# Kernel tuning notes

Measured on AMD Instinct MI355X. Metric: run time of the kernel, lower is better.

The kernel has to match this reference:

```python
import jax, jax.numpy as jnp
import numpy as np

N = 100000      # nodes
E = 1600000     # directed edges (before self-loops)
DIN = 128       # input feature dim
HID = 32        # per-head hidden dim
HEADS = 4
D1 = HID * HEADS  # 128, concat width
NG = 64         # graphs in batch
NEG_SLOPE = 0.2 # PyG GATConv leaky_relu slope


def setup_inputs() -> dict:
    key = jax.random.key(0)
    ks = jax.random.split(key, 16)
    s = 0.05
    x = jax.random.normal(ks[0], (N, DIN), dtype=jnp.float32)
    edge_index = jax.random.randint(ks[1], (2, E), 0, N, dtype=jnp.int32)
    batch = jnp.sort(jax.random.randint(ks[2], (N,), 0, NG, dtype=jnp.int32))
    # GATConv 1: in=DIN, out=HID, heads=HEADS, concat=True
    W1 = jax.random.normal(ks[3], (D1, DIN), dtype=jnp.float32) * s
    a1s = jax.random.normal(ks[4], (HEADS, HID), dtype=jnp.float32) * s
    a1d = jax.random.normal(ks[5], (HEADS, HID), dtype=jnp.float32) * s
    b1 = jnp.zeros((D1,), jnp.float32)
    # GATConv 2: in=D1, out=HID, heads=HEADS, concat=True
    W2 = jax.random.normal(ks[6], (D1, D1), dtype=jnp.float32) * s
    a2s = jax.random.normal(ks[7], (HEADS, HID), dtype=jnp.float32) * s
    a2d = jax.random.normal(ks[8], (HEADS, HID), dtype=jnp.float32) * s
    b2 = jnp.zeros((D1,), jnp.float32)
    # GATConv 3: in=D1, out=HID, heads=HEADS, concat=False (mean over heads)
    W3 = jax.random.normal(ks[9], (D1, D1), dtype=jnp.float32) * s
    a3s = jax.random.normal(ks[10], (HEADS, HID), dtype=jnp.float32) * s
    a3d = jax.random.normal(ks[11], (HEADS, HID), dtype=jnp.float32) * s
    b3 = jnp.zeros((HID,), jnp.float32)
    lin_w = jax.random.normal(ks[12], (1, HID), dtype=jnp.float32) * s
    lin_b = jnp.zeros((1,), jnp.float32)
    return {"x": x, "edge_index": edge_index, "batch": batch,
            "W1": W1, "a1s": a1s, "a1d": a1d, "b1": b1,
            "W2": W2, "a2s": a2s, "a2d": a2d, "b2": b2,
            "W3": W3, "a3s": a3s, "a3d": a3d, "b3": b3,
            "lin_w": lin_w, "lin_b": lin_b}


def _gat_conv(x, ei, W, att_src, att_dst, bias, concat):
    """PyG GATConv (no edge features, self-loops already in ei)."""
    n = x.shape[0]
    h = (x @ W.T).reshape(n, HEADS, HID)          # [N, H, C]
    src, dst = ei[0], ei[1]
    a_src = jnp.einsum('nhc,hc->nh', h, att_src)  # [N, H]
    a_dst = jnp.einsum('nhc,hc->nh', h, att_dst)
    e = jax.nn.leaky_relu(a_src[src] + a_dst[dst], NEG_SLOPE)  # [Etot, H]
    # segment softmax over incoming edges of each dst node
    e_max = jax.ops.segment_max(e, dst, num_segments=n)
    ex = jnp.exp(e - e_max[dst])
    denom = jax.ops.segment_sum(ex, dst, num_segments=n)
    alpha = ex / denom[dst]                        # [Etot, H]
    out = jax.ops.segment_sum(h[src] * alpha[:, :, None], dst, num_segments=n)
    if concat:
        out = out.reshape(n, HEADS * HID)
    else:
        out = out.mean(axis=1)
    return out + bias


def reference(x, edge_index, batch, W1, a1s, a1d, b1, W2, a2s, a2d, b2,
              W3, a3s, a3d, b3, lin_w, lin_b):
    loops = jnp.arange(N, dtype=edge_index.dtype)
    ei = jnp.concatenate([edge_index, jnp.stack([loops, loops])], axis=1)
    h = jax.nn.elu(_gat_conv(x, ei, W1, a1s, a1d, b1, True))
    h = jax.nn.elu(_gat_conv(h, ei, W2, a2s, a2d, b2, True))
    h = jax.nn.elu(_gat_conv(h, ei, W3, a3s, a3d, b3, False))
    h = h @ lin_w.T + lin_b                        # [N, 1]
    counts = jax.ops.segment_sum(jnp.ones((N,), h.dtype), batch, num_segments=NG)
    pooled = jax.ops.segment_sum(h, batch, num_segments=NG) / counts[:, None]
    return pooled.squeeze()                        # [NG]
```

## Files before the change

### kernel.cpp

```cpp
#include <hip/hip_runtime.h>
#include <hip/hip_fp16.h>
#include <math.h>

#define D1 128
#define NEG 0.2f
#define NODE_SHIFT 9
#define BIN_NODES 512
#define MAXBIN 256

typedef _Float16 v8h __attribute__((ext_vector_type(8)));
typedef float v4f __attribute__((ext_vector_type(4)));

__device__ __forceinline__ float lrelu(float v){ return v > 0.f ? v : NEG * v; }
__device__ __forceinline__ float elu_f(float v){ return v > 0.f ? v : __expf(v) - 1.f; }

__device__ __forceinline__ unsigned f2h2(float a, float b){
    return ((unsigned)__half_as_ushort(__float2half_rn(b)) << 16) |
           (unsigned)__half_as_ushort(__float2half_rn(a));
}
__device__ __forceinline__ float2 h2f2(unsigned u){
    float lo = __half2float(__ushort_as_half((unsigned short)(u & 0xffffu)));
    float hi = __half2float(__ushort_as_half((unsigned short)(u >> 16)));
    return make_float2(lo, hi);
}


__global__ __launch_bounds__(256) void kb_hist(const int* __restrict__ ei,
                                               int* __restrict__ binCnt,
                                               int n_edges, int etot, int nbin){
    __shared__ int h[MAXBIN];
    for (int i = threadIdx.x; i < nbin; i += 256) h[i] = 0;
    __syncthreads();
    int stride = gridDim.x * 256;
    for (int e = blockIdx.x * 256 + threadIdx.x; e < etot; e += stride){
        int dst = (e < n_edges) ? ei[n_edges + e] : (e - n_edges);
        atomicAdd(&h[dst >> NODE_SHIFT], 1);
    }
    __syncthreads();
    for (int i = threadIdx.x; i < nbin; i += 256)
        if (h[i]) atomicAdd(&binCnt[i], h[i]);
}

__global__ void kb_scan(const int* __restrict__ binCnt, int* __restrict__ binStart,
                        int* __restrict__ binCursor, int nbin,
                        int* __restrict__ rowptr, int n_nodes, int etot){
    if (threadIdx.x == 0){
        int run = 0;
        for (int b = 0; b < nbin; b++){
            binStart[b] = run; binCursor[b] = run; run += binCnt[b];
        }
        binStart[nbin] = run;
        rowptr[n_nodes] = etot;
    }
}

__global__ __launch_bounds__(256) void kb_scatter(const int* __restrict__ ei,
                                                  int* __restrict__ binCursor,
                                                  unsigned* __restrict__ staged,
                                                  int n_edges, int etot, int nbin){
    __shared__ int cnt[MAXBIN];
    __shared__ int base[MAXBIN];
    int e0 = blockIdx.x * 4096;
    for (int i = threadIdx.x; i < nbin; i += 256) cnt[i] = 0;
    __syncthreads();
    #pragma unroll 4
    for (int r = 0; r < 16; r++){
        int e = e0 + r * 256 + threadIdx.x;
        if (e < etot){
            int dst = (e < n_edges) ? ei[n_edges + e] : (e - n_edges);
            atomicAdd(&cnt[dst >> NODE_SHIFT], 1);
        }
    }
    __syncthreads();
    for (int i = threadIdx.x; i < nbin; i += 256){
        base[i] = cnt[i] ? atomicAdd(&binCursor[i], cnt[i]) : 0;
        cnt[i] = 0;
    }
    __syncthreads();
    #pragma unroll 4
    for (int r = 0; r < 16; r++){
        int e = e0 + r * 256 + threadIdx.x;
        if (e < etot){
            int src, dst;
            if (e < n_edges){ src = ei[e]; dst = ei[n_edges + e]; }
            else            { src = dst = e - n_edges; }
            int b = dst >> NODE_SHIFT;
            int p = base[b] + atomicAdd(&cnt[b], 1);
            staged[p] = ((unsigned)(dst & (BIN_NODES - 1)) << 17) | (unsigned)src;
        }
    }
}

__global__ __launch_bounds__(512) void kb_final(const unsigned* __restrict__ staged,
                                                const int* __restrict__ binStart,
                                                int* __restrict__ rowptr,
                                                int* __restrict__ eidx, int n_nodes){
    __shared__ int deg[BIN_NODES];
    __shared__ int cur[BIN_NODES];
    int b = blockIdx.x;
    int nbase = b << NODE_SHIFT;
    int s0 = binStart[b], s1 = binStart[b + 1];
    deg[threadIdx.x] = 0;
    __syncthreads();
    for (int i = s0 + threadIdx.x; i < s1; i += 512)
        atomicAdd(&deg[staged[i] >> 17], 1);
    __syncthreads();
    int v = deg[threadIdx.x];
    cur[threadIdx.x] = v;
    __syncthreads();
    for (int off = 1; off < BIN_NODES; off <<= 1){
        int t = (threadIdx.x >= off) ? cur[threadIdx.x - off] : 0;
        __syncthreads();
        cur[threadIdx.x] += t;
        __syncthreads();
    }
    int excl = cur[threadIdx.x] - v;
    int node = nbase + threadIdx.x;
    if (node < n_nodes) rowptr[node] = s0 + excl;
    cur[threadIdx.x] = s0 + excl;
    __syncthreads();
    for (int i = s0 + threadIdx.x; i < s1; i += 512){
        unsigned pr = staged[i];
        int p = atomicAdd(&cur[pr >> 17], 1);
        eidx[p] = (int)(pr & 0x1FFFFu);
    }
}


__global__ void k_prepw(const float* __restrict__ W1, const float* __restrict__ W2,
                        const float* __restrict__ W3, unsigned short* __restrict__ Bp){
    int t = blockIdx.x * 256 + threadIdx.x;
    if (t >= 49152) return;
    int w = t >> 14;
    int r = t & 16383;
    int k = r >> 7, j = r & 127;
    const float* W = (w == 0) ? W1 : (w == 1) ? W2 : W3;
    float val = W[j * 128 + k];
    int idx = (k >> 3) * 1024 + j * 8 + (k & 7);
    Bp[w * 16384 + idx] = __half_as_ushort(__float2half_rn(val));
}


template<int FP32SRC>
__global__ __launch_bounds__(256, 4) void k_mgemm(
        const float* __restrict__ Xf, const unsigned short* __restrict__ Xh,
        const unsigned short* __restrict__ Bp,
        const float* __restrict__ aw_s, const float* __restrict__ aw_d,
        unsigned short* __restrict__ Hh,
        float* __restrict__ asrc, float* __restrict__ adst, int n_rows){
    __shared__ unsigned short Bs[16384];
    int lane = threadIdx.x & 63;
    int wv   = threadIdx.x >> 6;
    int li = lane & 15, quad = lane >> 4;
    int r0 = blockIdx.x * 128 + wv * 32;

    int row0 = r0 + li;
    int row1 = r0 + 16 + li;
    int rc0 = row0 < n_rows ? row0 : 0;
    int rc1 = row1 < n_rows ? row1 : 0;

    v8h a0[4], a1[4];
    #pragma unroll
    for (int ks = 0; ks < 4; ks++){
        int koff = ks * 32 + quad * 8;
        if (FP32SRC){
            float f0[8], f1[8];
            *(float4*)&f0[0] = *(const float4*)(Xf + (size_t)rc0 * 128 + koff);
            *(float4*)&f0[4] = *(const float4*)(Xf + (size_t)rc0 * 128 + koff + 4);
            *(float4*)&f1[0] = *(const float4*)(Xf + (size_t)rc1 * 128 + koff);
            *(float4*)&f1[4] = *(const float4*)(Xf + (size_t)rc1 * 128 + koff + 4);
            #pragma unroll
            for (int i = 0; i < 8; i++){
                a0[ks][i] = (_Float16)f0[i];
                a1[ks][i] = (_Float16)f1[i];
            }
        } else {
            a0[ks] = *(const v8h*)(Xh + (size_t)rc0 * 128 + koff);
            a1[ks] = *(const v8h*)(Xh + (size_t)rc1 * 128 + koff);
        }
    }

    #pragma unroll
    for (int i = 0; i < 8; i++){
        int idx = threadIdx.x + i * 256;
        ((float4*)Bs)[idx] = ((const float4*)Bp)[idx];
    }
    __syncthreads();

    v4f acc[2][8];
    #pragma unroll
    for (int m = 0; m < 2; m++)
        #pragma unroll
        for (int t = 0; t < 8; t++)
            acc[m][t] = (v4f){0.f, 0.f, 0.f, 0.f};

    #pragma unroll
    for (int ks = 0; ks < 4; ks++){
        #pragma unroll
        for (int t = 0; t < 8; t++){
            int bo = (ks * 4 + quad) * 1024 + (t * 16 + li) * 8;
            v8h b = *(const v8h*)(Bs + bo);
            acc[0][t] = __builtin_amdgcn_mfma_f32_16x16x32_f16(a0[ks], b, acc[0][t], 0, 0, 0);
            acc[1][t] = __builtin_amdgcn_mfma_f32_16x16x32_f16(a1[ks], b, acc[1][t], 0, 0, 0);
        }
    }

    #pragma unroll
    for (int m = 0; m < 2; m++){
        #pragma unroll
        for (int t = 0; t < 8; t++){
            #pragma unroll
            for (int r = 0; r < 4; r++){
                float v  = acc[m][t][r];
                float vo = __shfl_xor(v, 1);
                if (!(li & 1)){
                    int row = r0 + m * 16 + quad * 4 + r;
                    if (row < n_rows)
                        *(unsigned*)(Hh + (size_t)row * 128 + t * 16 + li) = f2h2(v, vo);
                }
            }
        }
    }

    float as8[8], ad8[8];
    #pragma unroll
    for (int t = 0; t < 8; t++){
        as8[t] = aw_s[t * 16 + li];
        ad8[t] = aw_d[t * 16 + li];
    }
    #pragma unroll
    for (int m = 0; m < 2; m++){
        #pragma unroll
        for (int r = 0; r < 4; r++){
            float sp[4], dp[4];
            #pragma unroll
            for (int h = 0; h < 4; h++){
                sp[h] = acc[m][2*h][r] * as8[2*h] + acc[m][2*h+1][r] * as8[2*h+1];
                dp[h] = acc[m][2*h][r] * ad8[2*h] + acc[m][2*h+1][r] * ad8[2*h+1];
            }
            #pragma unroll
            for (int off = 1; off < 16; off <<= 1){
                #pragma unroll
                for (int h = 0; h < 4; h++){
                    sp[h] += __shfl_xor(sp[h], off);
                    dp[h] += __shfl_xor(dp[h], off);
                }
            }
            if (li == 0){
                int row = r0 + m * 16 + quad * 4 + r;
                if (row < n_rows){
                    ((float4*)asrc)[row] = make_float4(sp[0], sp[1], sp[2], sp[3]);
                    ((float4*)adst)[row] = make_float4(dp[0], dp[1], dp[2], dp[3]);
                }
            }
        }
    }
}


template<int MEAN>
__global__ __launch_bounds__(256) void k_aggr(
        const unsigned* __restrict__ Hh,
        const float* __restrict__ asrc, const float* __restrict__ adst,
        const int* __restrict__ rowptr, const int* __restrict__ eidx,
        const float* __restrict__ bias,
        unsigned short* __restrict__ O, float* __restrict__ Of, int n_nodes){
    int lane = threadIdx.x & 63;
    int wid  = threadIdx.x >> 6;
    int n = blockIdx.x * 4 + wid;
    if (n >= n_nodes) return;
    int row0 = rowptr[n];
    int deg  = rowptr[n + 1] - row0;
    const int* ep = eidx + row0;
    unsigned hd = (unsigned)(lane >> 4);
    unsigned ul = (unsigned)lane;
    float4 ad = ((const float4*)adst)[n];
    float adh = hd == 0 ? ad.x : hd == 1 ? ad.y : hd == 2 ? ad.z : ad.w;
    unsigned wh = (ul >> 3) & 3;
    float adw = wh == 0 ? ad.x : wh == 1 ? ad.y : wh == 2 ? ad.z : ad.w;
    int wsrc = (int)(hd * 8);

    float accx = 0.f, accy = 0.f, den = 0.f;
    int i = 0;
    for (; i + 8 <= deg; i += 8){
        unsigned s[8];
        #pragma unroll
        for (int j = 0; j < 8; j++) s[j] = (unsigned)ep[i + j];
        float aW = asrc[s[ul & 7] * 4u + wh];
        float w = __expf(lrelu(aW + adw));
        unsigned hw[8];
        #pragma unroll
        for (int j = 0; j < 8; j++) hw[j] = Hh[s[j] * 64u + ul];
        #pragma unroll
        for (int j = 0; j < 8; j++){
            float wj = __shfl(w, wsrc + j);
            float2 hv = h2f2(hw[j]);
            den  += wj;
            accx += wj * hv.x;
            accy += wj * hv.y;
        }
    }
    for (; i < deg; i++){
        unsigned s = (unsigned)ep[i];
        float w = __expf(lrelu(asrc[s * 4u + hd] + adh));
        float2 hv = h2f2(Hh[s * 64u + ul]);
        den  += w;
        accx += w * hv.x;
        accy += w * hv.y;
    }
    float rdh = 1.f / den;
    accx *= rdh; accy *= rdh;

    int c = lane * 2;
    if (!MEAN){
        float ox = elu_f(accx + bias[c]);
        float oy = elu_f(accy + bias[c + 1]);
        *(unsigned*)(O + (size_t)n * 128 + c) = f2h2(ox, oy);
    } else {
        float sx = accx, sy = accy;
        sx += __shfl_xor(sx, 16); sy += __shfl_xor(sy, 16);
        sx += __shfl_xor(sx, 32); sy += __shfl_xor(sy, 32);
        if (lane < 16){
            int cc = lane * 2;
            float ox = elu_f(sx * 0.25f + bias[cc]);
            float oy = elu_f(sy * 0.25f + bias[cc + 1]);
            *(float2*)(Of + (size_t)n * 32 + cc) = make_float2(ox, oy);
        }
    }
}


__global__ void k_readout(const float* __restrict__ H3, const int* __restrict__ batch,
                          const float* __restrict__ lw, const float* __restrict__ lb,
                          float* __restrict__ pool, float* __restrict__ cnt, int n_nodes){
    __shared__ float pl[64];
    __shared__ float cl[64];
    if (threadIdx.x < 64){ pl[threadIdx.x] = 0.f; cl[threadIdx.x] = 0.f; }
    __syncthreads();
    int n = blockIdx.x * 256 + threadIdx.x;
    if (n < n_nodes){
        const float4* hp = (const float4*)(H3 + (size_t)n * 32);
        const float4* wp = (const float4*)lw;
        float y = 0.f;
        #pragma unroll
        for (int i = 0; i < 8; i++){
            float4 h4 = hp[i], w4 = wp[i];
            y += h4.x * w4.x + h4.y * w4.y + h4.z * w4.z + h4.w * w4.w;
        }
        y += lb[0];
        int b = batch[n];
        atomicAdd(&pl[b], y);
        atomicAdd(&cl[b], 1.f);
    }
    __syncthreads();
    if (threadIdx.x < 64 && cl[threadIdx.x] != 0.f){
        atomicAdd(&pool[threadIdx.x], pl[threadIdx.x]);
        atomicAdd(&cnt[threadIdx.x], cl[threadIdx.x]);
    }
}

__global__ void k_final(const float* __restrict__ pool, const float* __restrict__ cnt,
                        float* __restrict__ out){
    int g = threadIdx.x;
    if (g < 64) out[g] = (cnt[g] > 0.f) ? pool[g] / cnt[g] : 0.f;
}


extern "C" void kernel_launch(void* const* d_in, const int* in_sizes, int n_in,
                              void* d_out, int out_size, void* d_ws, size_t ws_size,
                              hipStream_t stream){
    const float* x   = (const float*)d_in[0];
    const int*   ei  = (const int*)  d_in[1];
    const int*   bat = (const int*)  d_in[2];
    const float* W1  = (const float*)d_in[3];
    const float* a1s = (const float*)d_in[4];
    const float* a1d = (const float*)d_in[5];
    const float* b1  = (const float*)d_in[6];
    const float* W2  = (const float*)d_in[7];
    const float* a2s = (const float*)d_in[8];
    const float* a2d = (const float*)d_in[9];
    const float* b2  = (const float*)d_in[10];
    const float* W3  = (const float*)d_in[11];
    const float* a3s = (const float*)d_in[12];
    const float* a3d = (const float*)d_in[13];
    const float* b3  = (const float*)d_in[14];
    const float* lw  = (const float*)d_in[15];
    const float* lb  = (const float*)d_in[16];
    (void)n_in; (void)out_size; (void)ws_size;

    const int n_nodes = in_sizes[0] / D1;
    const int n_edges = in_sizes[1] / 2;
    const int etot    = n_edges + n_nodes;
    const int nbin    = (n_nodes + BIN_NODES - 1) >> NODE_SHIFT;

    char* p = (char*)d_ws;
    size_t off = 0;
    auto alloc = [&](size_t bytes) -> char* {
        char* r = p + off;
        off = (off + bytes + 511) & ~(size_t)511;
        return r;
    };
    unsigned short* Hh   = (unsigned short*)alloc((size_t)n_nodes * 128 * 2);
    unsigned short* Xh   = (unsigned short*)alloc((size_t)n_nodes * 128 * 2);
    float*          asrc = (float*)alloc((size_t)n_nodes * 4 * 4);
    float*          adst = (float*)alloc((size_t)n_nodes * 4 * 4);
    unsigned short* Bp   = (unsigned short*)alloc(3 * 16384 * 2);
    int*      rowptr  = (int*)alloc((size_t)(n_nodes + 1) * 4);
    int*      eidx    = (int*)alloc((size_t)etot * 4);
    unsigned* staged  = (unsigned*)alloc((size_t)etot * 4);
    int*      binCnt  = (int*)alloc(MAXBIN * 4);
    int*      binStart= (int*)alloc((MAXBIN + 1) * 4);
    int*      binCur  = (int*)alloc(MAXBIN * 4);
    float*    pool    = (float*)alloc(64 * 4);
    float*    cnt     = (float*)alloc(64 * 4);
    float*    h3      = (float*)Xh;

    hipMemsetAsync(binCnt, 0, MAXBIN * 4, stream);
    hipMemsetAsync(pool, 0, 64 * 4, stream);
    hipMemsetAsync(cnt, 0, 64 * 4, stream);

    k_prepw<<<192, 256, 0, stream>>>(W1, W2, W3, Bp);

    int cb = (etot + 4095) / 4096;
    kb_hist<<<cb, 256, 0, stream>>>(ei, binCnt, n_edges, etot, nbin);
    kb_scan<<<1, 64, 0, stream>>>(binCnt, binStart, binCur, nbin, rowptr, n_nodes, etot);
    kb_scatter<<<cb, 256, 0, stream>>>(ei, binCur, staged, n_edges, etot, nbin);
    kb_final<<<nbin, 512, 0, stream>>>(staged, binStart, rowptr, eidx, n_nodes);

    int mb = (n_nodes + 127) / 128;
    int rb = (n_nodes + 3) / 4;

    k_mgemm<1><<<mb, 256, 0, stream>>>(x, nullptr, Bp,
                                       a1s, a1d, Hh, asrc, adst, n_nodes);
    k_aggr<0><<<rb, 256, 0, stream>>>((const unsigned*)Hh, asrc, adst, rowptr, eidx,
                                      b1, Xh, nullptr, n_nodes);
    k_mgemm<0><<<mb, 256, 0, stream>>>(nullptr, Xh, Bp + 16384,
                                       a2s, a2d, Hh, asrc, adst, n_nodes);
    k_aggr<0><<<rb, 256, 0, stream>>>((const unsigned*)Hh, asrc, adst, rowptr, eidx,
                                      b2, Xh, nullptr, n_nodes);
    k_mgemm<0><<<mb, 256, 0, stream>>>(nullptr, Xh, Bp + 32768,
                                       a3s, a3d, Hh, asrc, adst, n_nodes);
    k_aggr<1><<<rb, 256, 0, stream>>>((const unsigned*)Hh, asrc, adst, rowptr, eidx,
                                      b3, nullptr, h3, n_nodes);

    int ob = (n_nodes + 255) / 256;
    k_readout<<<ob, 256, 0, stream>>>(h3, bat, lw, lb, pool, cnt, n_nodes);
    k_final<<<1, 64, 0, stream>>>(pool, cnt, (float*)d_out);
}
```

Measured before the change: 520.6 us.

## Restructure GAT aggregation to compute 16 edges x 4 heads weights per wave

The aggregation kernel now has each lane compute one (edge, head) attention weight for a chunk of 16 edges, instead of 8 edges with redundant lanes. Source indices are broadcast with readlane, so the gather addresses are wave-uniform. Weights are distributed with ds_bpermute, and the denominator is reduced across lanes once at the end. The remainder is handled with a masked chunk plus a software-prefetched tail loop. This cuts redundant exp and asrc loads and per-edge scalar index loads, at the cost of more cross-lane operations and extra tail-path code.

```diff
diff --git a/kernel.cpp b/kernel.cpp
--- a/kernel.cpp
+++ b/kernel.cpp
@@ -258,6 +258,12 @@
 }
 
 
+__device__ __forceinline__ void acc2(float wj, unsigned u, float& ax, float& ay){
+    __half2 h = *(__half2*)&u;
+    ax = fmaf(wj, __half2float(h.x), ax);
+    ay = fmaf(wj, __half2float(h.y), ay);
+}
+
 template<int MEAN>
 __global__ __launch_bounds__(256) void k_aggr(
         const unsigned* __restrict__ Hh,
@@ -267,47 +273,79 @@
         unsigned short* __restrict__ O, float* __restrict__ Of, int n_nodes){
     int lane = threadIdx.x & 63;
     int wid  = threadIdx.x >> 6;
-    int n = blockIdx.x * 4 + wid;
+    int n = __builtin_amdgcn_readfirstlane(blockIdx.x * 4 + wid);
     if (n >= n_nodes) return;
     int row0 = rowptr[n];
     int deg  = rowptr[n + 1] - row0;
     const int* ep = eidx + row0;
-    unsigned hd = (unsigned)(lane >> 4);
-    unsigned ul = (unsigned)lane;
+    int ul = lane;
+    int eh = ul & 3;
+    int ej = ul >> 2;
+    int hd = ul >> 4;
+    int bp = hd << 2;
     float4 ad = ((const float4*)adst)[n];
-    float adh = hd == 0 ? ad.x : hd == 1 ? ad.y : hd == 2 ? ad.z : ad.w;
-    unsigned wh = (ul >> 3) & 3;
-    float adw = wh == 0 ? ad.x : wh == 1 ? ad.y : wh == 2 ? ad.z : ad.w;
-    int wsrc = (int)(hd * 8);
-
-    float accx = 0.f, accy = 0.f, den = 0.f;
+    float adw = eh == 0 ? ad.x : eh == 1 ? ad.y : eh == 2 ? ad.z : ad.w;
+
+    float accx = 0.f, accy = 0.f, denp = 0.f;
     int i = 0;
-    for (; i + 8 <= deg; i += 8){
-        unsigned s[8];
-        #pragma unroll
-        for (int j = 0; j < 8; j++) s[j] = (unsigned)ep[i + j];
-        float aW = asrc[s[ul & 7] * 4u + wh];
-        float w = __expf(lrelu(aW + adw));
-        unsigned hw[8];
-        #pragma unroll
-        for (int j = 0; j < 8; j++) hw[j] = Hh[s[j] * 64u + ul];
-        #pragma unroll
-        for (int j = 0; j < 8; j++){
-            float wj = __shfl(w, wsrc + j);
-            float2 hv = h2f2(hw[j]);
-            den  += wj;
-            accx += wj * hv.x;
-            accy += wj * hv.y;
-        }
-    }
-    for (; i < deg; i++){
-        unsigned s = (unsigned)ep[i];
-        float w = __expf(lrelu(asrc[s * 4u + hd] + adh));
-        float2 hv = h2f2(Hh[s * 64u + ul]);
-        den  += w;
-        accx += w * hv.x;
-        accy += w * hv.y;
-    }
+
+    for (; i + 16 <= deg; i += 16){
+        int sv = ep[i + ej];
+        float aW = asrc[(size_t)(unsigned)sv * 4u + (unsigned)eh];
+        float t = aW + adw;
+        float w = __expf(fmaxf(t, NEG * t));
+        denp += w;
+        int wi = __float_as_int(w);
+        #pragma unroll
+        for (int j = 0; j < 16; j++){
+            int sj = __builtin_amdgcn_readlane(sv, j * 4);
+            unsigned hwj = Hh[(size_t)(unsigned)sj * 64u + (unsigned)ul];
+            float wj = __int_as_float(__builtin_amdgcn_ds_bpermute(bp + (j << 4), wi));
+            acc2(wj, hwj, accx, accy);
+        }
+    }
+
+    int r = deg - i;
+    if (r > 0){
+        int jj = (ej < r) ? (i + ej) : i;
+        int sv = ep[jj];
+        float aW = asrc[(size_t)(unsigned)sv * 4u + (unsigned)eh];
+        float t = aW + adw;
+        float w = (ej < r) ? __expf(fmaxf(t, NEG * t)) : 0.f;
+        denp += w;
+        int wi = __float_as_int(w);
+        int j = 0;
+        if (r >= 8){
+            #pragma unroll
+            for (int q = 0; q < 8; q++){
+                int sj = __builtin_amdgcn_readlane(sv, q * 4);
+                unsigned hwj = Hh[(size_t)(unsigned)sj * 64u + (unsigned)ul];
+                float wj = __int_as_float(__builtin_amdgcn_ds_bpermute(bp + (q << 4), wi));
+                acc2(wj, hwj, accx, accy);
+            }
+            j = 8;
+        }
+        if (j < r){
+            int sj = __builtin_amdgcn_readlane(sv, j * 4);
+            unsigned hw_c = Hh[(size_t)(unsigned)sj * 64u + (unsigned)ul];
+            for (; j < r; j++){
+                unsigned hw_n = 0u;
+                if (j + 1 < r){
+                    int sn = __builtin_amdgcn_readlane(sv, (j + 1) * 4);
+                    hw_n = Hh[(size_t)(unsigned)sn * 64u + (unsigned)ul];
+                }
+                float wj = __int_as_float(__builtin_amdgcn_ds_bpermute(bp + (j << 4), wi));
+                acc2(wj, hw_c, accx, accy);
+                hw_c = hw_n;
+            }
+        }
+    }
+
+    denp += __shfl_xor(denp, 4);
+    denp += __shfl_xor(denp, 8);
+    denp += __shfl_xor(denp, 16);
+    denp += __shfl_xor(denp, 32);
+    float den = __int_as_float(__builtin_amdgcn_ds_bpermute(bp, __float_as_int(denp)));
     float rdh = 1.f / den;
     accx *= rdh; accy *= rdh;
 
```

Measured after the change: 483.0 us. 1.08x faster.

## Restructure GAT aggregation to process four edges per wave with 16-byte gathers

Applied to the files above, without the earlier changes.

Rewrites the per-node aggregation kernel so that each wave computes attention weights for up to 32 edges at once, one edge-head pair per lane. Four edges are then gathered in parallel, with each group of 16 lanes loading a full 256-byte fp16 feature row as uint4 chunks. Gathers for the second half of a chunk are software-pipelined behind the accumulation of the first half. Partial sums are reduced across lane groups with shuffles at the end, and occupancy is raised with launch bounds. The aim is fewer, wider memory transactions and less serialization over edges, at the cost of extra cross-lane permutes and reductions.

```diff
diff --git a/kernel.cpp b/kernel.cpp
--- a/kernel.cpp
+++ b/kernel.cpp
@@ -258,8 +258,18 @@
 }
 
 
+__device__ __forceinline__ void cons4(uint4 hv, float w, float* acc){
+    unsigned u[4] = {hv.x, hv.y, hv.z, hv.w};
+    #pragma unroll
+    for (int q = 0; q < 4; q++){
+        float2 f = h2f2(u[q]);
+        acc[2*q]   = fmaf(w, f.x, acc[2*q]);
+        acc[2*q+1] = fmaf(w, f.y, acc[2*q+1]);
+    }
+}
+
 template<int MEAN>
-__global__ __launch_bounds__(256) void k_aggr(
+__global__ __launch_bounds__(256, 8) void k_aggr(
         const unsigned* __restrict__ Hh,
         const float* __restrict__ asrc, const float* __restrict__ adst,
         const int* __restrict__ rowptr, const int* __restrict__ eidx,
@@ -267,64 +277,130 @@
         unsigned short* __restrict__ O, float* __restrict__ Of, int n_nodes){
     int lane = threadIdx.x & 63;
     int wid  = threadIdx.x >> 6;
-    int n = blockIdx.x * 4 + wid;
+    int n = __builtin_amdgcn_readfirstlane(blockIdx.x * 4 + wid);
     if (n >= n_nodes) return;
     int row0 = rowptr[n];
     int deg  = rowptr[n + 1] - row0;
     const int* ep = eidx + row0;
-    unsigned hd = (unsigned)(lane >> 4);
-    unsigned ul = (unsigned)lane;
+    int l  = lane;
+    int eh = l & 3;
+    int ej = l >> 2;
+    int m  = l & 15;
+    int wb = l & 60;
+    int hb = l & 12;
     float4 ad = ((const float4*)adst)[n];
-    float adh = hd == 0 ? ad.x : hd == 1 ? ad.y : hd == 2 ? ad.z : ad.w;
-    unsigned wh = (ul >> 3) & 3;
-    float adw = wh == 0 ? ad.x : wh == 1 ? ad.y : wh == 2 ? ad.z : ad.w;
-    int wsrc = (int)(hd * 8);
-
-    float accx = 0.f, accy = 0.f, den = 0.f;
-    int i = 0;
-    for (; i + 8 <= deg; i += 8){
-        unsigned s[8];
-        #pragma unroll
-        for (int j = 0; j < 8; j++) s[j] = (unsigned)ep[i + j];
-        float aW = asrc[s[ul & 7] * 4u + wh];
-        float w = __expf(lrelu(aW + adw));
-        unsigned hw[8];
-        #pragma unroll
-        for (int j = 0; j < 8; j++) hw[j] = Hh[s[j] * 64u + ul];
-        #pragma unroll
-        for (int j = 0; j < 8; j++){
-            float wj = __shfl(w, wsrc + j);
-            float2 hv = h2f2(hw[j]);
-            den  += wj;
-            accx += wj * hv.x;
-            accy += wj * hv.y;
-        }
-    }
-    for (; i < deg; i++){
-        unsigned s = (unsigned)ep[i];
-        float w = __expf(lrelu(asrc[s * 4u + hd] + adh));
-        float2 hv = h2f2(Hh[s * 64u + ul]);
-        den  += w;
-        accx += w * hv.x;
-        accy += w * hv.y;
-    }
+    float adw = eh == 0 ? ad.x : eh == 1 ? ad.y : eh == 2 ? ad.z : ad.w;
+
+    const uint4* H4 = (const uint4*)Hh;
+    float acc[8];
+    #pragma unroll
+    for (int q = 0; q < 8; q++) acc[q] = 0.f;
+    float denp = 0.f;
+
+    for (int i = 0; i < deg; i += 32){
+        int rem = deg - i; if (rem > 32) rem = 32;
+        int last = i + rem - 1;
+        int j0 = i + ej;
+        int sv0 = ep[j0 < last ? j0 : last];
+        float t0 = asrc[(size_t)(unsigned)sv0 * 4u + (unsigned)eh] + adw;
+        float w0f = __expf(fmaxf(t0, NEG * t0));
+        float w0 = (ej < rem) ? w0f : 0.f;
+        denp += w0;
+        int w0i = __float_as_int(w0);
+
+        if (rem <= 16){
+            uint4 hv[4];
+            #pragma unroll
+            for (int t = 0; t < 4; t++){
+                int svt = __builtin_amdgcn_ds_bpermute((t << 6) + wb, sv0);
+                hv[t] = H4[(unsigned)svt * 16u + (unsigned)m];
+            }
+            #pragma unroll
+            for (int t = 0; t < 4; t++){
+                float wt = __int_as_float(__builtin_amdgcn_ds_bpermute((t << 6) + wb, w0i));
+                cons4(hv[t], wt, acc);
+            }
+        } else {
+            int j1 = i + 16 + ej;
+            int sv1 = ep[j1 < last ? j1 : last];
+            float t1 = asrc[(size_t)(unsigned)sv1 * 4u + (unsigned)eh] + adw;
+            float w1f = __expf(fmaxf(t1, NEG * t1));
+            float w1 = (16 + ej < rem) ? w1f : 0.f;
+            denp += w1;
+            int w1i = __float_as_int(w1);
+
+            uint4 hv[4];
+            #pragma unroll
+            for (int t = 0; t < 4; t++){
+                int svt = __builtin_amdgcn_ds_bpermute((t << 6) + wb, sv0);
+                hv[t] = H4[(unsigned)svt * 16u + (unsigned)m];
+            }
+            #pragma unroll
+            for (int t = 0; t < 4; t++){
+                float wt = __int_as_float(__builtin_amdgcn_ds_bpermute((t << 6) + wb, w0i));
+                uint4 cur = hv[t];
+                int svt = __builtin_amdgcn_ds_bpermute((t << 6) + wb, sv1);
+                hv[t] = H4[(unsigned)svt * 16u + (unsigned)m];
+                cons4(cur, wt, acc);
+            }
+            #pragma unroll
+            for (int t = 0; t < 4; t++){
+                float wt = __int_as_float(__builtin_amdgcn_ds_bpermute((t << 6) + wb, w1i));
+                cons4(hv[t], wt, acc);
+            }
+        }
+    }
+
+    #pragma unroll
+    for (int q = 0; q < 8; q++){
+        acc[q] += __shfl_xor(acc[q], 16);
+        acc[q] += __shfl_xor(acc[q], 32);
+    }
+    denp += __shfl_xor(denp, 4);
+    denp += __shfl_xor(denp, 8);
+    denp += __shfl_xor(denp, 16);
+    denp += __shfl_xor(denp, 32);
+    float den = __int_as_float(__builtin_amdgcn_ds_bpermute(hb, __float_as_int(denp)));
     float rdh = 1.f / den;
-    accx *= rdh; accy *= rdh;
-
-    int c = lane * 2;
+
     if (!MEAN){
-        float ox = elu_f(accx + bias[c]);
-        float oy = elu_f(accy + bias[c + 1]);
-        *(unsigned*)(O + (size_t)n * 128 + c) = f2h2(ox, oy);
+        if (l < 16){
+            float4 b0 = *(const float4*)(bias + m * 8);
+            float4 b1 = *(const float4*)(bias + m * 8 + 4);
+            float e0 = elu_f(acc[0] * rdh + b0.x);
+            float e1 = elu_f(acc[1] * rdh + b0.y);
+            float e2 = elu_f(acc[2] * rdh + b0.z);
+            float e3 = elu_f(acc[3] * rdh + b0.w);
+            float e4 = elu_f(acc[4] * rdh + b1.x);
+            float e5 = elu_f(acc[5] * rdh + b1.y);
+            float e6 = elu_f(acc[6] * rdh + b1.z);
+            float e7 = elu_f(acc[7] * rdh + b1.w);
+            uint4 ov;
+            ov.x = f2h2(e0, e1); ov.y = f2h2(e2, e3);
+            ov.z = f2h2(e4, e5); ov.w = f2h2(e6, e7);
+            *(uint4*)(O + (size_t)n * 128 + m * 8) = ov;
+        }
     } else {
-        float sx = accx, sy = accy;
-        sx += __shfl_xor(sx, 16); sy += __shfl_xor(sy, 16);
-        sx += __shfl_xor(sx, 32); sy += __shfl_xor(sy, 32);
-        if (lane < 16){
-            int cc = lane * 2;
-            float ox = elu_f(sx * 0.25f + bias[cc]);
-            float oy = elu_f(sy * 0.25f + bias[cc + 1]);
-            *(float2*)(Of + (size_t)n * 32 + cc) = make_float2(ox, oy);
+        float v[8];
+        #pragma unroll
+        for (int q = 0; q < 8; q++) v[q] = acc[q] * rdh;
+        #pragma unroll
+        for (int q = 0; q < 8; q++){
+            v[q] += __shfl_xor(v[q], 4);
+            v[q] += __shfl_xor(v[q], 8);
+        }
+        if (l < 4){
+            float4 o0, o1;
+            o0.x = elu_f(v[0] * 0.25f + bias[l * 8 + 0]);
+            o0.y = elu_f(v[1] * 0.25f + bias[l * 8 + 1]);
+            o0.z = elu_f(v[2] * 0.25f + bias[l * 8 + 2]);
+            o0.w = elu_f(v[3] * 0.25f + bias[l * 8 + 3]);
+            o1.x = elu_f(v[4] * 0.25f + bias[l * 8 + 4]);
+            o1.y = elu_f(v[5] * 0.25f + bias[l * 8 + 5]);
+            o1.z = elu_f(v[6] * 0.25f + bias[l * 8 + 6]);
+            o1.w = elu_f(v[7] * 0.25f + bias[l * 8 + 7]);
+            *(float4*)(Of + (size_t)n * 32 + l * 8)     = o0;
+            *(float4*)(Of + (size_t)n * 32 + l * 8 + 4) = o1;
         }
     }
 }
```

Result: faster. 487.8 us (-6.3%).
